# Kernel optimization log

Measured on AMD Instinct MI355X. Metric: run time of the kernel, lower is better.

The kernel has to match this reference:

```python
import jax, jax.numpy as jnp
import numpy as np

B, N, D, H = 4, 1024, 1024, 16
DH = D // H
MLP = 4 * D
EPS = 1e-6


def setup_inputs() -> dict:
    key = jax.random.key(0)
    ks = jax.random.split(key, 16)
    s = lambda fan_in: 1.0 / np.sqrt(fan_in)
    inp = {
        "x": jax.random.normal(ks[0], (B, N, D), jnp.float32),
        "c": jax.random.normal(ks[1], (B, D), jnp.float32),
        # weights stored (in, out); torch Linear is x @ W.T + b
        "Wq": jax.random.normal(ks[2], (D, D), jnp.float32) * s(D),
        "bq": jnp.zeros((D,), jnp.float32),
        "Wkv": jax.random.normal(ks[3], (D, 2 * D), jnp.float32) * s(D),
        "bkv": jnp.zeros((2 * D,), jnp.float32),
        "Wo": jax.random.normal(ks[4], (D, D), jnp.float32) * s(D),
        "bo": jnp.zeros((D,), jnp.float32),
        "W1": jax.random.normal(ks[5], (D, MLP), jnp.float32) * s(D),
        "b1": jnp.zeros((MLP,), jnp.float32),
        "W2": jax.random.normal(ks[6], (MLP, D), jnp.float32) * s(MLP),
        "b2": jnp.zeros((D,), jnp.float32),
        "Wada": jax.random.normal(ks[7], (D, 6 * D), jnp.float32) * s(D),
        "bada": jnp.zeros((6 * D,), jnp.float32),
    }
    return inp


def _layernorm(h):
    mu = jnp.mean(h, axis=-1, keepdims=True)
    var = jnp.mean(jnp.square(h - mu), axis=-1, keepdims=True)
    return (h - mu) / jnp.sqrt(var + EPS)


def _modulate(h, shift, scale):
    return h * (1.0 + scale[:, None, :]) + shift[:, None, :]


def reference(x, c, Wq, bq, Wkv, bkv, Wo, bo, W1, b1, W2, b2, Wada, bada):
    scale = DH ** -0.5
    mod = jax.nn.silu(c) @ Wada + bada  # [B, 6D]
    sh_msa, sc_msa, g_msa, sh_mlp, sc_mlp, g_mlp = jnp.split(mod, 6, axis=-1)

    # --- attention branch ---
    h = _modulate(_layernorm(x), sh_msa, sc_msa)
    q = (h @ Wq + bq).reshape(B, N, H, DH)
    kv = h @ Wkv + bkv
    k, v = jnp.split(kv, 2, axis=-1)
    k = k.reshape(B, N, H, DH)
    v = v.reshape(B, N, H, DH)
    sim = jnp.einsum("bihd,bjhd->bhij", q, k) * scale  # [B,H,N,N]
    attn = jax.nn.softmax(sim, axis=-1)
    out = jnp.einsum("bhij,bjhd->bihd", attn, v).reshape(B, N, D)
    out = out @ Wo + bo
    x = x + g_msa[:, None, :] * out

    # --- MLP branch ---
    h2 = _modulate(_layernorm(x), sh_mlp, sc_mlp)
    m = jax.nn.gelu(h2 @ W1 + b1, approximate=True) @ W2 + b2
    x = x + g_mlp[:, None, :] * m
    return x
```

## Files before the change

### kernel.cpp

```cpp
#include <hip/hip_runtime.h>
#include <hip/hip_bf16.h>
#include <cstdint>

typedef __attribute__((ext_vector_type(4))) float f32x4;
typedef __attribute__((ext_vector_type(16))) float f32x16;
typedef __attribute__((ext_vector_type(8))) short s16x8;
typedef __attribute__((ext_vector_type(4))) unsigned u32x4;
typedef unsigned short u16;

#define B_  4
#define N_  1024
#define D_  1024
#define H_  16
#define DH_ 64
#define M_  4096
#define SIXD 6144

#define WAITV(n) asm volatile("s_waitcnt vmcnt(" #n ")" ::: "memory")

__device__ __forceinline__ u16 f2bf(float f) {
    unsigned u = __builtin_bit_cast(unsigned, f);
    unsigned r = (u + 0x7fffu + ((u >> 16) & 1u)) >> 16;
    return (u16)r;
}

__device__ __forceinline__ unsigned cvtpk(float a, float b) {
    unsigned r;
    asm("v_cvt_pk_bf16_f32 %0, %1, %2" : "=v"(r) : "v"(a), "v"(b));
    return r;
}

__device__ __forceinline__ void gload16(const void* g, void* l) {
    __builtin_amdgcn_global_load_lds((const __attribute__((address_space(1))) void*)g,
                                     (__attribute__((address_space(3))) void*)l,
                                     16, 0, 0);
}

__global__ __launch_bounds__(256) void transpose_all(const float* __restrict__ Wq,
                                                     const float* __restrict__ Wkv,
                                                     const float* __restrict__ Wo,
                                                     const float* __restrict__ W1,
                                                     const float* __restrict__ W2,
                                                     u16* __restrict__ wqkvT,
                                                     u16* __restrict__ woT,
                                                     u16* __restrict__ w1T,
                                                     u16* __restrict__ w2T) {
    int id = blockIdx.x;
    const float* in; u16* outp; int R, C, loc;
    if (id < 1024)      { in = Wq;  outp = wqkvT;           R = 1024; C = 1024; loc = id; }
    else if (id < 3072) { in = Wkv; outp = wqkvT + 1048576; R = 1024; C = 2048; loc = id - 1024; }
    else if (id < 4096) { in = Wo;  outp = woT;             R = 1024; C = 1024; loc = id - 3072; }
    else if (id < 8192) { in = W1;  outp = w1T;             R = 1024; C = 4096; loc = id - 4096; }
    else                { in = W2;  outp = w2T;             R = 4096; C = 1024; loc = id - 8192; }
    int tpc = C >> 5;
    int bx = loc % tpc, by = loc / tpc;
    __shared__ float t[32][33];
    int tx = threadIdx.x & 31, ty = threadIdx.x >> 5;
    int r0 = by * 32, c0 = bx * 32;
#pragma unroll
    for (int i = 0; i < 4; ++i)
        t[ty + 8 * i][tx] = in[(size_t)(r0 + ty + 8 * i) * C + c0 + tx];
    __syncthreads();
#pragma unroll
    for (int i = 0; i < 4; ++i)
        outp[(size_t)(c0 + ty + 8 * i) * R + r0 + tx] = f2bf(t[tx][ty + 8 * i]);
}

__global__ __launch_bounds__(256) void modk(const float* __restrict__ c,
                                            const float* __restrict__ Wada,
                                            const float* __restrict__ bada,
                                            float* __restrict__ mod) {
    __shared__ float sc[D_];
    int b = blockIdx.y, tid = threadIdx.x;
    for (int i = tid; i < D_; i += 256) {
        float v = c[b * D_ + i];
        sc[i] = v / (1.f + __expf(-v));
    }
    __syncthreads();
    int col = blockIdx.x * 256 + tid;
    float a0 = 0.f, a1 = 0.f, a2 = 0.f, a3 = 0.f;
    for (int k = 0; k < D_; k += 4) {
        a0 = fmaf(sc[k + 0], Wada[(size_t)(k + 0) * SIXD + col], a0);
        a1 = fmaf(sc[k + 1], Wada[(size_t)(k + 1) * SIXD + col], a1);
        a2 = fmaf(sc[k + 2], Wada[(size_t)(k + 2) * SIXD + col], a2);
        a3 = fmaf(sc[k + 3], Wada[(size_t)(k + 3) * SIXD + col], a3);
    }
    mod[b * SIXD + col] = bada[col] + ((a0 + a1) + (a2 + a3));
}

__global__ __launch_bounds__(256) void ln_mod(const float* __restrict__ x,
                                              const float* __restrict__ mod,
                                              int shift_c, int scale_c,
                                              u16* __restrict__ h) {
    int row = blockIdx.x;
    int b = row >> 10;
    int tid = threadIdx.x, w = tid >> 6;
    float4 xv = ((const float4*)(x + (size_t)row * D_))[tid];
    float s  = xv.x + xv.y + xv.z + xv.w;
    float s2 = xv.x * xv.x + xv.y * xv.y + xv.z * xv.z + xv.w * xv.w;
#pragma unroll
    for (int m = 1; m <= 32; m <<= 1) { s += __shfl_xor(s, m); s2 += __shfl_xor(s2, m); }
    __shared__ float red[8];
    if ((tid & 63) == 0) { red[w * 2] = s; red[w * 2 + 1] = s2; }
    __syncthreads();
    float S  = red[0] + red[2] + red[4] + red[6];
    float S2 = red[1] + red[3] + red[5] + red[7];
    float mu = S * (1.f / D_);
    float var = S2 * (1.f / D_) - mu * mu;
    float rstd = rsqrtf(var + 1e-6f);
    int d0 = tid * 4;
    float4 shv = *(const float4*)(mod + b * SIXD + shift_c * D_ + d0);
    float4 scv = *(const float4*)(mod + b * SIXD + scale_c * D_ + d0);
    ushort4 o;
    o.x = f2bf((xv.x - mu) * rstd * (1.f + scv.x) + shv.x);
    o.y = f2bf((xv.y - mu) * rstd * (1.f + scv.y) + shv.y);
    o.z = f2bf((xv.z - mu) * rstd * (1.f + scv.z) + shv.z);
    o.w = f2bf((xv.w - mu) * rstd * (1.f + scv.w) + shv.w);
    *(ushort4*)(h + (size_t)row * D_ + d0) = o;
}

template <int EPI>
__global__ __launch_bounds__(256) void gemm_bt(const u16* __restrict__ A,
                                               const u16* __restrict__ Bt,
                                               const float* __restrict__ bias,
                                               void* __restrict__ out,
                                               const float* __restrict__ xres,
                                               const float* __restrict__ mod,
                                               int M, int Nn, int K, int gate_c) {
    __shared__ char lds[2][32768];
    const int tid = threadIdx.x;
    const int w = tid >> 6, lane = tid & 63;
    const int li = lane & 15, lg = lane >> 4;
    const int nwg = gridDim.x * gridDim.y;
    const int flat = blockIdx.y * gridDim.x + blockIdx.x;
    const int wg = (flat & 7) * (nwg >> 3) + (flat >> 3);
    const int m0 = (wg / gridDim.x) * 128, n0 = (wg % gridDim.x) * 128;
    const int wr = w >> 1, wc = w & 1;

    f32x4 acc[4][4];
#pragma unroll
    for (int i = 0; i < 4; ++i)
#pragma unroll
        for (int j = 0; j < 4; ++j) acc[i][j] = (f32x4){0.f, 0.f, 0.f, 0.f};

    auto STAGE = [&](int kk, char* buf) {
#pragma unroll
        for (int j = 0; j < 8; ++j) {
            int basec = j * 256 + w * 64;
            int idx = basec + lane;
            int idl = idx & 1023;
            int row = idl >> 3, cc = idl & 7;
            const u16* src;
            if (idx < 1024)
                src = A + (size_t)(m0 + row) * K + kk + ((cc ^ (row & 7)) << 3);
            else
                src = Bt + (size_t)(n0 + row) * K + kk + ((cc ^ (row & 7)) << 3);
            gload16(src, buf + basec * 16);
        }
    };

    const int nt = K >> 6;
    STAGE(0, lds[0]);
    __syncthreads();
    int cur = 0;
    for (int t = 0; t < nt; ++t) {
        if (t + 1 < nt) { STAGE((t + 1) << 6, lds[cur ^ 1]); WAITV(8); }
        else WAITV(0);
        __builtin_amdgcn_s_barrier();
        __builtin_amdgcn_sched_barrier(0);
        const char* Ab = lds[cur];
        const char* Bb = lds[cur] + 16384;
#pragma unroll
        for (int hh = 0; hh < 2; ++hh) {
            s16x8 af[4], bfr[4];
#pragma unroll
            for (int mi = 0; mi < 4; ++mi) {
                int r = wr * 64 + mi * 16 + li;
                af[mi] = *(const s16x8*)(Ab + r * 128 + (((hh * 4 + lg) ^ (r & 7)) << 4));
            }
#pragma unroll
            for (int nj = 0; nj < 4; ++nj) {
                int r = wc * 64 + nj * 16 + li;
                bfr[nj] = *(const s16x8*)(Bb + r * 128 + (((hh * 4 + lg) ^ (r & 7)) << 4));
            }
#pragma unroll
            for (int mi = 0; mi < 4; ++mi)
#pragma unroll
                for (int nj = 0; nj < 4; ++nj)
                    acc[mi][nj] = __builtin_amdgcn_mfma_f32_16x16x32_bf16(
                        af[mi], bfr[nj], acc[mi][nj], 0, 0, 0);
        }
        __builtin_amdgcn_s_barrier();
        cur ^= 1;
    }

#pragma unroll
    for (int mi = 0; mi < 4; ++mi) {
#pragma unroll
        for (int nj = 0; nj < 4; ++nj) {
            int col = n0 + wc * 64 + nj * 16 + li;
            float bv = bias[col];
#pragma unroll
            for (int rg = 0; rg < 4; ++rg) {
                int grow = m0 + wr * 64 + mi * 16 + 4 * lg + rg;
                float v = acc[mi][nj][rg] + bv;
                int b = grow >> 10;
                size_t off = (size_t)grow * D_ + col;
                float g = mod[b * SIXD + gate_c * D_ + col];
                ((float*)out)[off] = xres[off] + g * v;
            }
        }
    }
}

template <int EPI>
__global__ __launch_bounds__(512, 2) void gemm256(const u16* __restrict__ A,
                                                  const u16* __restrict__ Bt,
                                                  const float* __restrict__ bias,
                                                  const float* __restrict__ bias2,
                                                  void* __restrict__ out,
                                                  int M, int Nn, int K,
                                                  int cm, int cn) {
    __shared__ char lds[2][65536];
    const int tid = threadIdx.x;
    const int w = tid >> 6, lane = tid & 63;
    const int li = lane & 15, lg = lane >> 4;
    const int wr = w >> 1, wc = w & 1;

    const int flat = blockIdx.x;
    const int xcd = flat & 7, r_ = flat >> 3;
    const int ntn = Nn >> 8;
    const int ncc = ntn / cn;
    const int mt = (xcd / ncc) * cm + (r_ % cm);
    const int nt_ = (xcd % ncc) * cn + (r_ / cm);
    const int m0 = mt * 256, n0 = nt_ * 256;

    f32x4 acc[4][8];
#pragma unroll
    for (int i = 0; i < 4; ++i)
#pragma unroll
        for (int j = 0; j < 8; ++j) acc[i][j] = (f32x4){0.f, 0.f, 0.f, 0.f};

    auto STAGE = [&](int kk, char* buf) {
#pragma unroll
        for (int j = 0; j < 4; ++j) {
            int basec = j * 512 + w * 64;
            int idx = basec + lane;
            int row = idx >> 3, cc = idx & 7;
            gload16(A + (size_t)(m0 + row) * K + kk + ((cc ^ (row & 7)) << 3),
                    buf + basec * 16);
            gload16(Bt + (size_t)(n0 + row) * K + kk + ((cc ^ (row & 7)) << 3),
                    buf + 32768 + basec * 16);
        }
    };

    const int nt = K >> 6;
    STAGE(0, lds[0]);
    __syncthreads();
    int cur = 0;
    for (int t = 0; t < nt; ++t) {
        if (t + 1 < nt) { STAGE((t + 1) << 6, lds[cur ^ 1]); WAITV(8); }
        else WAITV(0);
        __builtin_amdgcn_s_barrier();
        __builtin_amdgcn_sched_barrier(0);
        const char* Ab = lds[cur];
        const char* Bb = lds[cur] + 32768;
#pragma unroll
        for (int hh = 0; hh < 2; ++hh) {
            s16x8 af[4], bfr[8];
#pragma unroll
            for (int mi = 0; mi < 4; ++mi) {
                int r = wr * 64 + mi * 16 + li;
                af[mi] = *(const s16x8*)(Ab + r * 128 + (((hh * 4 + lg) ^ (r & 7)) << 4));
            }
#pragma unroll
            for (int nj = 0; nj < 8; ++nj) {
                int r = wc * 128 + nj * 16 + li;
                bfr[nj] = *(const s16x8*)(Bb + r * 128 + (((hh * 4 + lg) ^ (r & 7)) << 4));
            }
#pragma unroll
            for (int mi = 0; mi < 4; ++mi)
#pragma unroll
                for (int nj = 0; nj < 8; ++nj)
                    acc[mi][nj] = __builtin_amdgcn_mfma_f32_16x16x32_bf16(
                        af[mi], bfr[nj], acc[mi][nj], 0, 0, 0);
        }
        __builtin_amdgcn_s_barrier();
        cur ^= 1;
    }

#pragma unroll
    for (int nj = 0; nj < 8; ++nj) {
        int col = n0 + wc * 128 + nj * 16 + li;
        float bv;
        if (EPI == 5) bv = (col < D_) ? bias[col] : bias2[col - D_];
        else bv = bias[col];
#pragma unroll
        for (int mi = 0; mi < 4; ++mi) {
#pragma unroll
            for (int rg = 0; rg < 4; ++rg) {
                int grow = m0 + wr * 64 + mi * 16 + 4 * lg + rg;
                float v = acc[mi][nj][rg] + bv;
                if (EPI == 3) {
                    float u = 0.7978845608028654f * v * (1.f + 0.044715f * v * v);
                    u = fminf(fmaxf(u, -15.f), 15.f);
                    float e = __expf(2.f * u);
                    float th = (e - 1.f) / (e + 1.f);
                    ((u16*)out)[(size_t)grow * (size_t)Nn + col] = f2bf(0.5f * v * (1.f + th));
                } else {
                    int b = grow >> 10, n = grow & 1023;
                    if (n0 < 1024) {
                        int hd = col >> 6, dh = col & 63;
                        ((u16*)out)[(((size_t)(b * H_ + hd)) * N_ + n) * DH_ + dh] = f2bf(v);
                    } else if (n0 < 2048) {
                        int c2 = col - 1024;
                        int hd = c2 >> 6, dh = c2 & 63;
                        ((u16*)out)[4194304u + (((size_t)(b * H_ + hd)) * N_ + n) * DH_ + dh] =
                            f2bf(v);
                    } else {
                        int c2 = col - 2048;
                        int hd = c2 >> 6, dh = c2 & 63;
                        ((u16*)out)[8388608u + (((size_t)(b * H_ + hd)) * DH_ + dh) * N_ + n] =
                            f2bf(v);
                    }
                }
            }
        }
    }
}

__global__ __launch_bounds__(256) void attn2(const u16* __restrict__ q,
                                             const u16* __restrict__ k,
                                             const u16* __restrict__ vt,
                                             u16* __restrict__ o) {
    __shared__ __align__(16) char qs[16384];
    __shared__ __align__(16) char kv[2][16384];
    const int tid = threadIdx.x, w = tid >> 6, lane = tid & 63;
    const int l31 = lane & 31, hi = lane >> 5;
    const int flat = blockIdx.x;
    const int wgs = (flat & 7) * 64 + (flat >> 3);
    const int bh = wgs >> 3, qt = wgs & 7;
    const size_t base = (size_t)bh * (N_ * DH_);
    const int q0 = qt * 128;

#pragma unroll
    for (int j = 0; j < 4; ++j) {
        int basec = j * 256 + w * 64;
        int idx = basec + lane;
        int row = idx >> 3, cc = idx & 7;
        gload16(q + base + (size_t)(q0 + row) * DH_ + ((cc ^ (row & 7)) << 3),
                qs + basec * 16);
    }
    auto STAGEKV = [&](int t, char* buf) {
#pragma unroll
        for (int j = 0; j < 4; ++j) {
            int basec = j * 256 + w * 64;
            int idx = basec + lane;
            if (idx < 512) {
                int row = idx >> 3, cc = idx & 7;
                gload16(k + base + (size_t)(t * 64 + row) * DH_ + ((cc ^ (row & 7)) << 3),
                        buf + basec * 16);
            } else {
                int i2 = idx - 512;
                int row = i2 >> 3, cc = i2 & 7;
                gload16(vt + base + (size_t)row * N_ + t * 64 + ((cc ^ (row & 7)) << 3),
                        buf + basec * 16);
            }
        }
    };
    STAGEKV(0, kv[0]);
    __syncthreads();

    s16x8 qf[4];
    const int qr = w * 32 + l31;
#pragma unroll
    for (int st = 0; st < 4; ++st)
        qf[st] = *(const s16x8*)(qs + qr * 128 + (((st * 2 + hi) ^ (qr & 7)) << 4));

    f32x16 oa[2];
#pragma unroll
    for (int r = 0; r < 16; ++r) { oa[0][r] = 0.f; oa[1][r] = 0.f; }
    float mrow = -3e38f, lrow = 0.f;
    const float CSC = 0.125f * 1.44269504088896f;

    int cur = 0;
    for (int t = 0; t < 16; ++t) {
        if (t + 1 < 16) { STAGEKV(t + 1, kv[cur ^ 1]); WAITV(4); }
        else WAITV(0);
        __builtin_amdgcn_s_barrier();
        __builtin_amdgcn_sched_barrier(0);
        const char* Kb = kv[cur];
        const char* Vb = kv[cur] + 8192;

        f32x16 s[2];
#pragma unroll
        for (int r = 0; r < 16; ++r) { s[0][r] = 0.f; s[1][r] = 0.f; }
#pragma unroll
        for (int st = 0; st < 4; ++st) {
#pragma unroll
            for (int ks = 0; ks < 2; ++ks) {
                int r = ks * 32 + l31;
                s16x8 ka = *(const s16x8*)(Kb + r * 128 + (((st * 2 + hi) ^ (r & 7)) << 4));
                s[ks] = __builtin_amdgcn_mfma_f32_32x32x16_bf16(ka, qf[st], s[ks], 0, 0, 0);
            }
        }

        float tmax = s[0][0];
#pragma unroll
        for (int r = 1; r < 16; ++r) tmax = fmaxf(tmax, s[0][r]);
#pragma unroll
        for (int r = 0; r < 16; ++r) tmax = fmaxf(tmax, s[1][r]);
        tmax = fmaxf(tmax, __shfl_xor(tmax, 32));
        float mn = fmaxf(mrow, tmax);
        float al = __builtin_amdgcn_exp2f((mrow - mn) * CSC);
        float nmc = -mn * CSC;
        float rs0 = 0.f, rs1 = 0.f;
#pragma unroll
        for (int r = 0; r < 16; ++r) {
            float p0 = __builtin_amdgcn_exp2f(fmaf(s[0][r], CSC, nmc));
            float p1 = __builtin_amdgcn_exp2f(fmaf(s[1][r], CSC, nmc));
            s[0][r] = p0; s[1][r] = p1;
            rs0 += p0; rs1 += p1;
        }
        float rs = rs0 + rs1;
        rs += __shfl_xor(rs, 32);
        lrow = lrow * al + rs;
        mrow = mn;
#pragma unroll
        for (int r = 0; r < 16; ++r) { oa[0][r] *= al; oa[1][r] *= al; }

        unsigned u[16];
#pragma unroll
        for (int ks = 0; ks < 2; ++ks)
#pragma unroll
            for (int j = 0; j < 4; ++j) {
                u[ks * 8 + 2 * j]     = cvtpk(s[ks][4 * j + 0], s[ks][4 * j + 1]);
                u[ks * 8 + 2 * j + 1] = cvtpk(s[ks][4 * j + 2], s[ks][4 * j + 3]);
            }

#pragma unroll
        for (int kstep = 0; kstep < 4; ++kstep) {
            unsigned b0 = u[kstep * 4 + 0], b1 = u[kstep * 4 + 1];
            unsigned b2 = u[kstep * 4 + 2], b3 = u[kstep * 4 + 3];
            asm volatile("v_permlane32_swap_b32 %0, %1" : "+v"(b0), "+v"(b2));
            asm volatile("v_permlane32_swap_b32 %0, %1" : "+v"(b1), "+v"(b3));
            u32x4 pbu = (u32x4){b0, b1, b2, b3};
            s16x8 pb = __builtin_bit_cast(s16x8, pbu);
#pragma unroll
            for (int ds = 0; ds < 2; ++ds) {
                int r = ds * 32 + l31;
                s16x8 va = *(const s16x8*)(Vb + r * 128 + (((kstep * 2 + hi) ^ (r & 7)) << 4));
                oa[ds] = __builtin_amdgcn_mfma_f32_32x32x16_bf16(va, pb, oa[ds], 0, 0, 0);
            }
        }
        __builtin_amdgcn_s_barrier();
        cur ^= 1;
    }

    float inv = 1.f / lrow;
#pragma unroll
    for (int ds = 0; ds < 2; ++ds)
#pragma unroll
        for (int j = 0; j < 4; ++j)
#pragma unroll
            for (int t2 = 0; t2 < 2; ++t2) {
                unsigned pk = cvtpk(oa[ds][4 * j + 2 * t2] * inv,
                                    oa[ds][4 * j + 2 * t2 + 1] * inv);
                int row = qr;
                int dch = 4 * ds + j;
                *(unsigned*)(qs + row * 128 + ((dch ^ (row & 7)) << 4) +
                             (4 * hi + 2 * t2) * 2) = pk;
            }
    __syncthreads();
    {
        int r = tid >> 1, h2 = tid & 1;
        const int b = bh >> 4, hd = bh & 15;
        size_t obase = ((size_t)(b * N_ + q0 + r)) * D_ + hd * DH_;
#pragma unroll
        for (int c = 0; c < 4; ++c) {
            int c2 = h2 * 4 + c;
            s16x8 v = *(const s16x8*)(qs + r * 128 + ((c2 ^ (r & 7)) << 4));
            *(s16x8*)(o + obase + c2 * 8) = v;
        }
    }
}

extern "C" void kernel_launch(void* const* d_in, const int* in_sizes, int n_in,
                              void* d_out, int out_size, void* d_ws, size_t ws_size,
                              hipStream_t stream) {
    const float* x    = (const float*)d_in[0];
    const float* c    = (const float*)d_in[1];
    const float* Wq   = (const float*)d_in[2];
    const float* bq   = (const float*)d_in[3];
    const float* Wkv  = (const float*)d_in[4];
    const float* bkv  = (const float*)d_in[5];
    const float* Wo   = (const float*)d_in[6];
    const float* bo   = (const float*)d_in[7];
    const float* W1   = (const float*)d_in[8];
    const float* b1   = (const float*)d_in[9];
    const float* W2   = (const float*)d_in[10];
    const float* b2   = (const float*)d_in[11];
    const float* Wada = (const float*)d_in[12];
    const float* bada = (const float*)d_in[13];

    char* ws = (char*)d_ws;
    const size_t MB = 1024 * 1024;
    u16*   wqkvT = (u16*)(ws + 0);
    u16*   woT  = (u16*)(ws + 6 * MB);
    u16*   w1T  = (u16*)(ws + 8 * MB);
    u16*   w2T  = (u16*)(ws + 16 * MB);
    float* mod  = (float*)(ws + 24 * MB);
    u16*   h    = (u16*)(ws + 25 * MB);
    u16*   qb   = (u16*)(ws + 33 * MB);
    u16*   ao   = (u16*)(ws + 57 * MB);
    float* x1   = (float*)(ws + 65 * MB);
    u16*   m1   = (u16*)(ws + 33 * MB);
    float* outp = (float*)d_out;

    transpose_all<<<12288, 256, 0, stream>>>(Wq, Wkv, Wo, W1, W2, wqkvT, woT, w1T, w2T);

    modk<<<dim3(24, 4), 256, 0, stream>>>(c, Wada, bada, mod);
    ln_mod<<<M_, 256, 0, stream>>>(x, mod, 0, 1, h);

    gemm256<5><<<192, 512, 0, stream>>>(h, wqkvT, bq, bkv, qb, M_, 3 * D_, D_, 4, 6);

    attn2<<<512, 256, 0, stream>>>(qb, qb + 4194304, qb + 8388608, ao);

    gemm_bt<2><<<dim3(8, 32), 256, 0, stream>>>(ao, woT, bo, x1, x, mod, M_, D_, D_, 2);

    ln_mod<<<M_, 256, 0, stream>>>(x1, mod, 3, 4, h);

    gemm256<3><<<256, 512, 0, stream>>>(h, w1T, b1, nullptr, m1, M_, 4 * D_, D_, 4, 8);
    gemm_bt<4><<<dim3(8, 32), 256, 0, stream>>>(m1, w2T, b2, outp, x1, mod, M_, D_, 4 * D_, 5);
}
```

Measured before the change: 252.4 us.

## Restructure 256x256 GEMM into quadrant-pipelined schedule with staggered prefetch

Rewrites the 256x256 bf16 GEMM so each K step is split into four quadrant phases, each computing a 128x128 sub-tile. The loads for the next tiles are spread across the phases, with some prefetched two steps ahead into the current buffer. The warp layout changes from 4x2 to 2x4, and MFMA bursts are wrapped in s_setprio. The aim is to overlap global loads and LDS reads with MFMA work and smooth issue, at the cost of more barriers and more complex buffer-reuse hazards.

```diff
diff --git a/kernel.cpp b/kernel.cpp
--- a/kernel.cpp
+++ b/kernel.cpp
@@ -214,18 +214,18 @@
 }
 
 template <int EPI>
-__global__ __launch_bounds__(512, 2) void gemm256(const u16* __restrict__ A,
-                                                  const u16* __restrict__ Bt,
-                                                  const float* __restrict__ bias,
-                                                  const float* __restrict__ bias2,
-                                                  void* __restrict__ out,
-                                                  int M, int Nn, int K,
-                                                  int cm, int cn) {
-    __shared__ char lds[2][65536];
+__global__ __launch_bounds__(512, 2) void gemm256p(const u16* __restrict__ A,
+                                                   const u16* __restrict__ Bt,
+                                                   const float* __restrict__ bias,
+                                                   const float* __restrict__ bias2,
+                                                   void* __restrict__ out,
+                                                   int M, int Nn, int K,
+                                                   int cm, int cn) {
+    __shared__ __align__(16) char lds[131072];
     const int tid = threadIdx.x;
     const int w = tid >> 6, lane = tid & 63;
     const int li = lane & 15, lg = lane >> 4;
-    const int wr = w >> 1, wc = w & 1;
+    const int wr = w >> 2, wc = w & 3;
 
     const int flat = blockIdx.x;
     const int xcd = flat & 7, r_ = flat >> 3;
@@ -235,98 +235,131 @@
     const int nt_ = (xcd % ncc) * cn + (r_ / cm);
     const int m0 = mt * 256, n0 = nt_ * 256;
 
-    f32x4 acc[4][8];
-#pragma unroll
-    for (int i = 0; i < 4; ++i)
-#pragma unroll
-        for (int j = 0; j < 8; ++j) acc[i][j] = (f32x4){0.f, 0.f, 0.f, 0.f};
-
-    auto STAGE = [&](int kk, char* buf) {
-#pragma unroll
-        for (int j = 0; j < 4; ++j) {
-            int basec = j * 512 + w * 64;
-            int idx = basec + lane;
+    f32x4 acc[2][4][2][2];
+#pragma unroll
+    for (int a = 0; a < 2; ++a)
+#pragma unroll
+        for (int b = 0; b < 4; ++b)
+#pragma unroll
+            for (int c = 0; c < 2; ++c)
+#pragma unroll
+                for (int d = 0; d < 2; ++d) acc[a][b][c][d] = (f32x4){0.f, 0.f, 0.f, 0.f};
+
+    auto SH = [&](const u16* P, int rowbase, int kk, char* dst) {
+#pragma unroll
+        for (int j = 0; j < 2; ++j) {
+            int idx = j * 512 + w * 64 + lane;
             int row = idx >> 3, cc = idx & 7;
-            gload16(A + (size_t)(m0 + row) * K + kk + ((cc ^ (row & 7)) << 3),
-                    buf + basec * 16);
-            gload16(Bt + (size_t)(n0 + row) * K + kk + ((cc ^ (row & 7)) << 3),
-                    buf + 32768 + basec * 16);
+            gload16(P + (size_t)(rowbase + row) * K + kk + ((cc ^ (row & 7)) << 3),
+                    dst + (j * 512 + w * 64) * 16);
         }
     };
 
-    const int nt = K >> 6;
-    STAGE(0, lds[0]);
-    __syncthreads();
-    int cur = 0;
-    for (int t = 0; t < nt; ++t) {
-        if (t + 1 < nt) { STAGE((t + 1) << 6, lds[cur ^ 1]); WAITV(8); }
-        else WAITV(0);
-        __builtin_amdgcn_s_barrier();
-        __builtin_amdgcn_sched_barrier(0);
-        const char* Ab = lds[cur];
-        const char* Bb = lds[cur] + 32768;
-#pragma unroll
-        for (int hh = 0; hh < 2; ++hh) {
-            s16x8 af[4], bfr[8];
+    const int NT = K >> 6;
+    char* buf0 = lds;
+    char* buf1 = lds + 65536;
+    SH(A,  m0,       0, buf0 + 0);
+    SH(Bt, n0,       0, buf0 + 32768);
+    SH(A,  m0 + 128, 0, buf0 + 16384);
+    SH(Bt, n0 + 128, 0, buf0 + 49152);
+    SH(A,  m0,       64, buf1 + 0);
+    SH(Bt, n0,       64, buf1 + 32768);
+    SH(A,  m0 + 128, 64, buf1 + 16384);
+    WAITV(6);
+    __builtin_amdgcn_s_barrier();
+    __builtin_amdgcn_sched_barrier(0);
+
+    for (int T = 0; T < NT; ++T) {
+        char* cb = (T & 1) ? buf1 : buf0;
+        char* nb = (T & 1) ? buf0 : buf1;
+#pragma unroll
+        for (int p = 0; p < 4; ++p) {
+            const int qm = p >> 1, qn = p & 1;
+            const char* Ab = cb + qm * 16384;
+            const char* Bb = cb + 32768 + qn * 16384;
+            s16x8 af[4][2], bfx[2][2];
 #pragma unroll
             for (int mi = 0; mi < 4; ++mi) {
                 int r = wr * 64 + mi * 16 + li;
-                af[mi] = *(const s16x8*)(Ab + r * 128 + (((hh * 4 + lg) ^ (r & 7)) << 4));
-            }
-#pragma unroll
-            for (int nj = 0; nj < 8; ++nj) {
-                int r = wc * 128 + nj * 16 + li;
-                bfr[nj] = *(const s16x8*)(Bb + r * 128 + (((hh * 4 + lg) ^ (r & 7)) << 4));
-            }
-#pragma unroll
-            for (int mi = 0; mi < 4; ++mi)
-#pragma unroll
-                for (int nj = 0; nj < 8; ++nj)
-                    acc[mi][nj] = __builtin_amdgcn_mfma_f32_16x16x32_bf16(
-                        af[mi], bfr[nj], acc[mi][nj], 0, 0, 0);
-        }
-        __builtin_amdgcn_s_barrier();
-        cur ^= 1;
-    }
-
-#pragma unroll
-    for (int nj = 0; nj < 8; ++nj) {
-        int col = n0 + wc * 128 + nj * 16 + li;
-        float bv;
-        if (EPI == 5) bv = (col < D_) ? bias[col] : bias2[col - D_];
-        else bv = bias[col];
-#pragma unroll
-        for (int mi = 0; mi < 4; ++mi) {
-#pragma unroll
-            for (int rg = 0; rg < 4; ++rg) {
-                int grow = m0 + wr * 64 + mi * 16 + 4 * lg + rg;
-                float v = acc[mi][nj][rg] + bv;
-                if (EPI == 3) {
-                    float u = 0.7978845608028654f * v * (1.f + 0.044715f * v * v);
-                    u = fminf(fmaxf(u, -15.f), 15.f);
-                    float e = __expf(2.f * u);
-                    float th = (e - 1.f) / (e + 1.f);
-                    ((u16*)out)[(size_t)grow * (size_t)Nn + col] = f2bf(0.5f * v * (1.f + th));
-                } else {
-                    int b = grow >> 10, n = grow & 1023;
-                    if (n0 < 1024) {
-                        int hd = col >> 6, dh = col & 63;
-                        ((u16*)out)[(((size_t)(b * H_ + hd)) * N_ + n) * DH_ + dh] = f2bf(v);
-                    } else if (n0 < 2048) {
-                        int c2 = col - 1024;
-                        int hd = c2 >> 6, dh = c2 & 63;
-                        ((u16*)out)[4194304u + (((size_t)(b * H_ + hd)) * N_ + n) * DH_ + dh] =
-                            f2bf(v);
-                    } else {
-                        int c2 = col - 2048;
-                        int hd = c2 >> 6, dh = c2 & 63;
-                        ((u16*)out)[8388608u + (((size_t)(b * H_ + hd)) * DH_ + dh) * N_ + n] =
-                            f2bf(v);
+#pragma unroll
+                for (int ks = 0; ks < 2; ++ks)
+                    af[mi][ks] = *(const s16x8*)(Ab + r * 128 + (((ks * 4 + lg) ^ (r & 7)) << 4));
+            }
+#pragma unroll
+            for (int nj = 0; nj < 2; ++nj) {
+                int r = wc * 32 + nj * 16 + li;
+#pragma unroll
+                for (int ks = 0; ks < 2; ++ks)
+                    bfx[nj][ks] = *(const s16x8*)(Bb + r * 128 + (((ks * 4 + lg) ^ (r & 7)) << 4));
+            }
+            if (p == 0)      { if (T + 1 < NT) SH(Bt, n0 + 128, (T + 1) << 6, nb + 49152); }
+            else if (p == 1) { if (T + 2 < NT) SH(A,  m0,       (T + 2) << 6, cb + 0); }
+            else if (p == 2) { if (T + 2 < NT) SH(Bt, n0,      (T + 2) << 6, cb + 32768); }
+            else             { if (T + 2 < NT) SH(A,  m0 + 128, (T + 2) << 6, cb + 16384); }
+            __builtin_amdgcn_s_barrier();
+            asm volatile("s_waitcnt lgkmcnt(0)" ::: "memory");
+            __builtin_amdgcn_sched_barrier(0);
+            __builtin_amdgcn_s_setprio(1);
+#pragma unroll
+            for (int ks = 0; ks < 2; ++ks)
+#pragma unroll
+                for (int mi = 0; mi < 4; ++mi)
+#pragma unroll
+                    for (int nj = 0; nj < 2; ++nj)
+                        acc[qm][mi][qn][nj] = __builtin_amdgcn_mfma_f32_16x16x32_bf16(
+                            af[mi][ks], bfx[nj][ks], acc[qm][mi][qn][nj], 0, 0, 0);
+            __builtin_amdgcn_s_setprio(0);
+            if (p == 3) { if (T + 2 < NT) { WAITV(6); } else { WAITV(0); } }
+            __builtin_amdgcn_s_barrier();
+        }
+    }
+
+#pragma unroll
+    for (int qm = 0; qm < 2; ++qm)
+#pragma unroll
+        for (int qn = 0; qn < 2; ++qn)
+#pragma unroll
+            for (int nj = 0; nj < 2; ++nj) {
+                int col = n0 + qn * 128 + wc * 32 + nj * 16 + li;
+                float bv;
+                if (EPI == 5) bv = (col < D_) ? bias[col] : bias2[col - D_];
+                else bv = bias[col];
+#pragma unroll
+                for (int mi = 0; mi < 4; ++mi) {
+#pragma unroll
+                    for (int rg = 0; rg < 4; ++rg) {
+                        int grow = m0 + qm * 128 + wr * 64 + mi * 16 + 4 * lg + rg;
+                        float v = acc[qm][mi][qn][nj][rg] + bv;
+                        if (EPI == 3) {
+                            float u = 0.7978845608028654f * v * (1.f + 0.044715f * v * v);
+                            u = fminf(fmaxf(u, -15.f), 15.f);
+                            float e = __expf(2.f * u);
+                            float th = (e - 1.f) / (e + 1.f);
+                            ((u16*)out)[(size_t)grow * (size_t)Nn + col] =
+                                f2bf(0.5f * v * (1.f + th));
+                        } else {
+                            int b = grow >> 10, n = grow & 1023;
+                            if (col < D_) {
+                                int hd = col >> 6, dh = col & 63;
+                                ((u16*)out)[(((size_t)(b * H_ + hd)) * N_ + n) * DH_ + dh] =
+                                    f2bf(v);
+                            } else if (col < 2 * D_) {
+                                int c2 = col - D_;
+                                int hd = c2 >> 6, dh = c2 & 63;
+                                ((u16*)out)[4194304u +
+                                            (((size_t)(b * H_ + hd)) * N_ + n) * DH_ + dh] =
+                                    f2bf(v);
+                            } else {
+                                int c2 = col - 2 * D_;
+                                int hd = c2 >> 6, dh = c2 & 63;
+                                ((u16*)out)[8388608u +
+                                            (((size_t)(b * H_ + hd)) * DH_ + dh) * N_ + n] =
+                                    f2bf(v);
+                            }
+                        }
                     }
                 }
             }
-        }
-    }
 }
 
 __global__ __launch_bounds__(256) void attn2(const u16* __restrict__ q,
@@ -522,7 +555,7 @@
     modk<<<dim3(24, 4), 256, 0, stream>>>(c, Wada, bada, mod);
     ln_mod<<<M_, 256, 0, stream>>>(x, mod, 0, 1, h);
 
-    gemm256<5><<<192, 512, 0, stream>>>(h, wqkvT, bq, bkv, qb, M_, 3 * D_, D_, 4, 6);
+    gemm256p<5><<<192, 512, 0, stream>>>(h, wqkvT, bq, bkv, qb, M_, 3 * D_, D_, 4, 6);
 
     attn2<<<512, 256, 0, stream>>>(qb, qb + 4194304, qb + 8388608, ao);
 
@@ -530,6 +563,6 @@
 
     ln_mod<<<M_, 256, 0, stream>>>(x1, mod, 3, 4, h);
 
-    gemm256<3><<<256, 512, 0, stream>>>(h, w1T, b1, nullptr, m1, M_, 4 * D_, D_, 4, 8);
+    gemm256p<3><<<256, 512, 0, stream>>>(h, w1T, b1, nullptr, m1, M_, 4 * D_, D_, 4, 8);
     gemm_bt<4><<<dim3(8, 32), 256, 0, stream>>>(m1, w2T, b2, outp, x1, mod, M_, D_, 4 * D_, 5);
 }
```

Result: slower. 267.8 us (+6.1%).
